# Kernel tuning notes

Hardware: AMD Instinct MI355X
Metric: run time of the kernel (lower is better)

Reference implementation:

```python
import jax, jax.numpy as jnp
import numpy as np

B, S, D = 4, 1024, 1024
H, G = 16, 8            # num_heads, num_query_groups
HD = D // H             # head_dim = 64
E, TOPK, ED = 8, 2, 2 * D   # experts, top_k, expert_dim
GH = D // 2             # gate hidden
EPS = 1e-5


def setup_inputs() -> dict:
    key = jax.random.key(0)
    ks = iter(jax.random.split(key, 32))
    rn = lambda shape, s=0.02: jax.random.normal(next(ks), shape, jnp.float32) * s
    return {
        "x": jax.random.normal(next(ks), (B, S, D), jnp.float32),
        # GQA projections (stored [in, out])
        "wq": rn((D, G * HD)), "bq": jnp.zeros((G * HD,), jnp.float32),
        "wk": rn((D, D)), "bk": jnp.zeros((D,), jnp.float32),
        "wv": rn((D, D)), "bv": jnp.zeros((D,), jnp.float32),
        "wo": rn((D, D)), "bo": jnp.zeros((D,), jnp.float32),
        # LayerNorms
        "ln1_g": jnp.ones((D,), jnp.float32), "ln1_b": jnp.zeros((D,), jnp.float32),
        "ln2_g": jnp.ones((D,), jnp.float32), "ln2_b": jnp.zeros((D,), jnp.float32),
        # MoE gate: Linear(D, D//2) -> ReLU -> Linear(D//2, E)
        "gw1": rn((D, GH)), "gb1": jnp.zeros((GH,), jnp.float32),
        "gw2": rn((GH, E)), "gb2": jnp.zeros((E,), jnp.float32),
        # stacked expert FFNs: Linear(D, ED) -> GELU -> Linear(ED, D)
        "ew1": rn((E, D, ED)), "eb1": jnp.zeros((E, ED), jnp.float32),
        "ew2": rn((E, ED, D)), "eb2": jnp.zeros((E, D), jnp.float32),
    }


def _layernorm(x, g, b):
    mu = jnp.mean(x, axis=-1, keepdims=True)
    var = jnp.var(x, axis=-1, keepdims=True)
    return (x - mu) * jax.lax.rsqrt(var + EPS) * g + b


def _block(x, wq, bq, wk, bk, wv, bv, wo, bo, ln1_g, ln1_b, ln2_g, ln2_b,
           gw1, gb1, gw2, gb2, ew1, eb1, ew2, eb2):
    # --- GQA self-attention (dropout is identity in eval) ---
    h = _layernorm(x, ln1_g, ln1_b)
    q = (h @ wq + bq).reshape(B, S, G, HD).transpose(0, 2, 1, 3)   # [B,G,S,hd]
    k = (h @ wk + bk).reshape(B, S, H, HD).transpose(0, 2, 1, 3)   # [B,H,S,hd]
    v = (h @ wv + bv).reshape(B, S, H, HD).transpose(0, 2, 1, 3)
    q = jnp.repeat(q, H // G, axis=1)                              # repeat_interleave -> [B,H,S,hd]
    scores = jnp.einsum("bhqd,bhkd->bhqk", q, k) * (HD ** -0.5)
    attn = jax.nn.softmax(scores, axis=-1)
    ao = jnp.einsum("bhqk,bhkd->bhqd", attn, v)
    ao = ao.transpose(0, 2, 1, 3).reshape(B, S, D) @ wo + bo
    x = x + ao

    # --- MoE FFN ---
    h2 = _layernorm(x, ln2_g, ln2_b).reshape(-1, D)                # [T,D], T=B*S
    gate_logits = jax.nn.relu(h2 @ gw1 + gb1) @ gw2 + gb2          # [T,E]
    gate_w = jax.nn.softmax(gate_logits, axis=-1)
    top_w, top_i = jax.lax.top_k(gate_w, TOPK)                     # [T,k]
    top_w = jax.nn.softmax(top_w, axis=-1)                         # renormalize among top-k
    combine = jnp.sum(jax.nn.one_hot(top_i, E, dtype=h2.dtype) * top_w[..., None], axis=1)  # [T,E]
    hid = jax.nn.gelu(jnp.einsum("td,edh->teh", h2, ew1) + eb1, approximate=False)          # [T,E,ED]
    expert_out = jnp.einsum("teh,ehd->ted", hid, ew2) + eb2        # [T,E,D]
    moe = jnp.einsum("ted,te->td", expert_out, combine).reshape(B, S, D)
    return x + moe


def reference(x, wq, bq, wk, bk, wv, bv, wo, bo, ln1_g, ln1_b, ln2_g, ln2_b,
              gw1, gb1, gw2, gb2, ew1, eb1, ew2, eb2):
    return _block(x, wq, bq, wk, bk, wv, bv, wo, bo, ln1_g, ln1_b, ln2_g, ln2_b,
                  gw1, gb1, gw2, gb2, ew1, eb1, ew2, eb2)
```

## Files before the change

kernel.cpp:

```cpp
#include <hip/hip_runtime.h>

typedef __bf16 bf16x8 __attribute__((ext_vector_type(8)));
typedef float f32x4 __attribute__((ext_vector_type(4)));
typedef unsigned int u32x4 __attribute__((ext_vector_type(4)));
typedef unsigned int u32x2 __attribute__((ext_vector_type(2)));

#define DEV static __device__ __forceinline__

DEV unsigned short f2bf(float f) {
  unsigned int u = __builtin_bit_cast(unsigned int, f);
  u += 0x7fffu + ((u >> 16) & 1u);
  return (unsigned short)(u >> 16);
}
DEV float bf2f(unsigned int hbits) { return __builtin_bit_cast(float, hbits << 16); }

DEV bf16x8 load_bf8(const unsigned short* p) {
  u32x4 u = *(const u32x4*)p;
  return __builtin_bit_cast(bf16x8, u);
}
DEV void unpack8(u32x4 u, float f[8]) {
  f[0] = bf2f(u.x & 0xffffu); f[1] = bf2f(u.x >> 16);
  f[2] = bf2f(u.y & 0xffffu); f[3] = bf2f(u.y >> 16);
  f[4] = bf2f(u.z & 0xffffu); f[5] = bf2f(u.z >> 16);
  f[6] = bf2f(u.w & 0xffffu); f[7] = bf2f(u.w >> 16);
}
DEV void gload_lds16(const void* g, void* l) {
  __builtin_amdgcn_global_load_lds((const __attribute__((address_space(1))) void*)g,
                                   (__attribute__((address_space(3))) void*)l, 16, 0, 0);
}
DEV f32x4 mfma16(bf16x8 a, bf16x8 b, f32x4 c) {
  return __builtin_amdgcn_mfma_f32_16x16x32_bf16(a, b, c, 0, 0, 0);
}

__global__ __launch_bounds__(256) void cm_transpose(
    const float* __restrict__ src, unsigned short* __restrict__ dst,
    int K, int N, long srcStrideE, long dstStrideE) {
  src += (long)blockIdx.z * srcStrideE;
  dst += (long)blockIdx.z * dstStrideE;
  __shared__ float t[32][33];
  const int n0 = blockIdx.x * 32, k0 = blockIdx.y * 32;
  const int tx = threadIdx.x & 31, ty = threadIdx.x >> 5;
#pragma unroll
  for (int j = 0; j < 4; ++j) {
    int k = k0 + ty + j * 8, n = n0 + tx;
    if (k < K && n < N) t[ty + j * 8][tx] = src[(long)k * N + n];
  }
  __syncthreads();
#pragma unroll
  for (int j = 0; j < 4; ++j) {
    int n = n0 + ty + j * 8, k = k0 + tx;
    if (n < N && k < K) dst[(long)n * K + k] = f2bf(t[tx][ty + j * 8]);
  }
}

__global__ __launch_bounds__(256) void cm_transpose_split(
    const float* __restrict__ src, unsigned short* __restrict__ dhi,
    unsigned short* __restrict__ dlo, int K, int N) {
  __shared__ float t[32][33];
  const int n0 = blockIdx.x * 32, k0 = blockIdx.y * 32;
  const int tx = threadIdx.x & 31, ty = threadIdx.x >> 5;
#pragma unroll
  for (int j = 0; j < 4; ++j) {
    int k = k0 + ty + j * 8, n = n0 + tx;
    if (k < K && n < N) t[ty + j * 8][tx] = src[(long)k * N + n];
  }
  __syncthreads();
#pragma unroll
  for (int j = 0; j < 4; ++j) {
    int n = n0 + ty + j * 8, k = k0 + tx;
    if (n < N && k < K) {
      float v = t[tx][ty + j * 8];
      unsigned short hi = f2bf(v);
      dhi[(long)n * K + k] = hi;
      dlo[(long)n * K + k] = f2bf(v - bf2f(hi));
    }
  }
}

template <bool WLO>
__global__ __launch_bounds__(256) void cm_ln(
    const float* __restrict__ x, const float* __restrict__ g, const float* __restrict__ b,
    unsigned short* __restrict__ ob, unsigned short* __restrict__ olo) {
  const int row = blockIdx.x, tid = threadIdx.x;
  const f32x4 v = *(const f32x4*)(x + (long)row * 1024 + tid * 4);
  float s1 = v[0] + v[1] + v[2] + v[3];
  float s2 = v[0] * v[0] + v[1] * v[1] + v[2] * v[2] + v[3] * v[3];
#pragma unroll
  for (int m = 32; m >= 1; m >>= 1) { s1 += __shfl_xor(s1, m); s2 += __shfl_xor(s2, m); }
  __shared__ float r1[4], r2[4];
  if ((tid & 63) == 0) { r1[tid >> 6] = s1; r2[tid >> 6] = s2; }
  __syncthreads();
  s1 = r1[0] + r1[1] + r1[2] + r1[3];
  s2 = r2[0] + r2[1] + r2[2] + r2[3];
  const float mean = s1 * (1.f / 1024.f);
  const float rs = rsqrtf(s2 * (1.f / 1024.f) - mean * mean + 1e-5f);
  const f32x4 gg = *(const f32x4*)(g + tid * 4);
  const f32x4 bb = *(const f32x4*)(b + tid * 4);
  float o[4];
  unsigned short hi[4];
#pragma unroll
  for (int i = 0; i < 4; ++i) {
    o[i] = (v[i] - mean) * rs * gg[i] + bb[i];
    hi[i] = f2bf(o[i]);
  }
  u32x2 pk;
  pk.x = (unsigned)hi[0] | ((unsigned)hi[1] << 16);
  pk.y = (unsigned)hi[2] | ((unsigned)hi[3] << 16);
  *(u32x2*)(ob + (long)row * 1024 + tid * 4) = pk;
  if (WLO) {
    u32x2 pl;
    pl.x = (unsigned)f2bf(o[0] - bf2f(hi[0])) | ((unsigned)f2bf(o[1] - bf2f(hi[1])) << 16);
    pl.y = (unsigned)f2bf(o[2] - bf2f(hi[2])) | ((unsigned)f2bf(o[3] - bf2f(hi[3])) << 16);
    *(u32x2*)(olo + (long)row * 1024 + tid * 4) = pl;
  }
}

enum { EP_BF16 = 0, EP_RELU = 1, EP_GELU = 2, EP_RES_F32 = 3 };

template <int EPI, int MODE>
__global__ __launch_bounds__(256, 2) void cm_gemm_bt(
    const unsigned short* __restrict__ A, int lda,
    const unsigned short* __restrict__ BT, long btStrideE, int ldb,
    const float* __restrict__ bias, int biasStrideE,
    const float* __restrict__ res,
    void* __restrict__ outp, int ldc,
    int M, int K,
    const int* __restrict__ cnt, const int* __restrict__ offs,
    const int* __restrict__ rowidx) {
  const int z = blockIdx.z;
  int valid = M, rowbase = 0;
  if (MODE > 0) {
    valid = cnt[z];
    if ((int)blockIdx.y * 128 >= valid) return;
    rowbase = offs[z];
    BT += (long)z * btStrideE;
    bias += (long)z * biasStrideE;
  }
  const int tid = threadIdx.x;
  const int brow = blockIdx.y * 128, bcol = blockIdx.x * 128;
  const int wid = tid >> 6, lane = tid & 63;
  const int wr = wid >> 1, wc = wid & 1;
  const int srow0 = tid >> 2, scol = (tid & 3) * 8;

  __shared__ __align__(16) unsigned short As[128 * 32];
  __shared__ __align__(16) unsigned short Bs[128 * 32];

  long asrc[2], bsrc[2];
#pragma unroll
  for (int i = 0; i < 2; ++i) {
    int m = brow + srow0 + i * 64;
    if (MODE == 0) {
      asrc[i] = (long)m * lda;
    } else {
      int p = m < valid ? m : valid - 1;
      if (MODE == 1) asrc[i] = (long)rowidx[z * 4096 + p] * lda;
      else           asrc[i] = (long)(rowbase + p) * lda;
    }
    bsrc[i] = (long)(bcol + srow0 + i * 64) * ldb;
  }

  f32x4 acc[4][4] = {};

  for (int k0 = 0; k0 < K; k0 += 32) {
#pragma unroll
    for (int i = 0; i < 2; ++i) {
      gload_lds16(A + asrc[i] + k0 + scol, &As[(srow0 + i * 64) * 32 + scol]);
      gload_lds16(BT + bsrc[i] + k0 + scol, &Bs[(srow0 + i * 64) * 32 + scol]);
    }
    __syncthreads();
    bf16x8 af[4], bfr[4];
#pragma unroll
    for (int m = 0; m < 4; ++m)
      af[m] = load_bf8(&As[(wr * 64 + m * 16 + (lane & 15)) * 32 + (lane >> 4) * 8]);
#pragma unroll
    for (int n = 0; n < 4; ++n)
      bfr[n] = load_bf8(&Bs[(wc * 64 + n * 16 + (lane & 15)) * 32 + (lane >> 4) * 8]);
#pragma unroll
    for (int m = 0; m < 4; ++m)
#pragma unroll
      for (int n = 0; n < 4; ++n)
        acc[m][n] = mfma16(af[m], bfr[n], acc[m][n]);
    __syncthreads();
  }

#pragma unroll
  for (int m = 0; m < 4; ++m) {
#pragma unroll
    for (int rr = 0; rr < 4; ++rr) {
      const int lrow = brow + wr * 64 + m * 16 + (lane >> 4) * 4 + rr;
      if (MODE > 0 && lrow >= valid) continue;
      const long orow = (long)(rowbase + lrow);
#pragma unroll
      for (int n = 0; n < 4; ++n) {
        const int gcol = bcol + wc * 64 + n * 16 + (lane & 15);
        float vv = acc[m][n][rr] + bias[gcol];
        if constexpr (EPI == EP_RELU) vv = fmaxf(vv, 0.f);
        if constexpr (EPI == EP_GELU) vv = 0.5f * vv * (1.f + erff(vv * 0.70710678f));
        if constexpr (EPI == EP_RES_F32)
          ((float*)outp)[orow * ldc + gcol] = vv + res[orow * ldc + gcol];
        else
          ((unsigned short*)outp)[orow * ldc + gcol] = f2bf(vv);
      }
    }
  }
}

__global__ __launch_bounds__(256, 2) void cm_gemm_gate(
    const unsigned short* __restrict__ Ah, const unsigned short* __restrict__ Al,
    const unsigned short* __restrict__ Bh, const unsigned short* __restrict__ Bl,
    const float* __restrict__ bias, float* __restrict__ C) {
  const int tid = threadIdx.x;
  const int brow = blockIdx.y * 128, bcol = blockIdx.x * 128;
  const int wid = tid >> 6, lane = tid & 63;
  const int wr = wid >> 1, wc = wid & 1;
  const int srow0 = tid >> 2, scol = (tid & 3) * 8;

  __shared__ __align__(16) unsigned short Ash[128 * 32], Asl[128 * 32];
  __shared__ __align__(16) unsigned short Bsh[128 * 32], Bsl[128 * 32];

  f32x4 acc[4][4] = {};

  for (int k0 = 0; k0 < 1024; k0 += 32) {
#pragma unroll
    for (int i = 0; i < 2; ++i) {
      const long ar = (long)(brow + srow0 + i * 64) * 1024 + k0 + scol;
      const long br = (long)(bcol + srow0 + i * 64) * 1024 + k0 + scol;
      const int lo = (srow0 + i * 64) * 32 + scol;
      gload_lds16(Ah + ar, &Ash[lo]);
      gload_lds16(Al + ar, &Asl[lo]);
      gload_lds16(Bh + br, &Bsh[lo]);
      gload_lds16(Bl + br, &Bsl[lo]);
    }
    __syncthreads();
    bf16x8 ah[4], al[4], bh[4], bl[4];
#pragma unroll
    for (int m = 0; m < 4; ++m) {
      const int ro = (wr * 64 + m * 16 + (lane & 15)) * 32 + (lane >> 4) * 8;
      ah[m] = load_bf8(&Ash[ro]); al[m] = load_bf8(&Asl[ro]);
    }
#pragma unroll
    for (int n = 0; n < 4; ++n) {
      const int ro = (wc * 64 + n * 16 + (lane & 15)) * 32 + (lane >> 4) * 8;
      bh[n] = load_bf8(&Bsh[ro]); bl[n] = load_bf8(&Bsl[ro]);
    }
#pragma unroll
    for (int m = 0; m < 4; ++m)
#pragma unroll
      for (int n = 0; n < 4; ++n) {
        acc[m][n] = mfma16(al[m], bh[n], acc[m][n]);
        acc[m][n] = mfma16(ah[m], bl[n], acc[m][n]);
        acc[m][n] = mfma16(ah[m], bh[n], acc[m][n]);
      }
    __syncthreads();
  }

#pragma unroll
  for (int m = 0; m < 4; ++m)
#pragma unroll
    for (int rr = 0; rr < 4; ++rr) {
      const long orow = brow + wr * 64 + m * 16 + (lane >> 4) * 4 + rr;
#pragma unroll
      for (int n = 0; n < 4; ++n) {
        const int gcol = bcol + wc * 64 + n * 16 + (lane & 15);
        C[orow * 512 + gcol] = fmaxf(acc[m][n][rr] + bias[gcol], 0.f);
      }
    }
}

__global__ __launch_bounds__(256) void cm_vtrans(
    const unsigned short* __restrict__ qkv, unsigned short* __restrict__ Vt) {
  const int stile = blockIdx.x, bh = blockIdx.y;
  const int b = bh >> 4, h = bh & 15;
  const int tid = threadIdx.x;
  __shared__ __align__(16) unsigned short t[64][72];
  const int d0 = (tid & 7) * 8, sl = tid >> 3;
#pragma unroll
  for (int i = 0; i < 2; ++i) {
    const int s = sl + i * 32;
    *(u32x4*)&t[s][d0] =
        *(const u32x4*)(qkv + (long)(b * 1024 + stile * 64 + s) * 2560 + 1536 + h * 64 + d0);
  }
  __syncthreads();
  const int s0 = (tid & 7) * 8, dl = tid >> 3;
#pragma unroll
  for (int i = 0; i < 2; ++i) {
    const int d = dl + i * 32;
    unsigned short vals[8];
#pragma unroll
    for (int j = 0; j < 8; ++j) vals[j] = t[s0 + j][d];
    u32x4 u;
    u.x = vals[0] | ((unsigned)vals[1] << 16);
    u.y = vals[2] | ((unsigned)vals[3] << 16);
    u.z = vals[4] | ((unsigned)vals[5] << 16);
    u.w = vals[6] | ((unsigned)vals[7] << 16);
    *(u32x4*)(Vt + (long)(bh * 64 + d) * 1024 + stile * 64 + s0) = u;
  }
}

__global__ __launch_bounds__(256, 2) void cm_attn(
    const unsigned short* __restrict__ qkv,
    const unsigned short* __restrict__ Vt,
    unsigned short* __restrict__ ao) {
  const int qt = blockIdx.x, bh = blockIdx.y;
  const int b = bh >> 4, h = bh & 15, g = h >> 1;
  const int tid = threadIdx.x, wid = tid >> 6, lane = tid & 63;
  const int q0 = qt * 32;

  __shared__ __align__(16) unsigned short sc[32][1032];
  __shared__ float rowrcp[32];

  bf16x8 bq[2][2];
#pragma unroll
  for (int nf = 0; nf < 2; ++nf)
#pragma unroll
    for (int ks = 0; ks < 2; ++ks)
      bq[nf][ks] = load_bf8(qkv + (long)(b * 1024 + q0 + nf * 16 + (lane & 15)) * 2560 +
                            g * 64 + ks * 32 + (lane >> 4) * 8);

#pragma unroll 1
  for (int c = 0; c < 4; ++c) {
    const int kb = wid * 256 + c * 64;
    f32x4 acc[4][2] = {};
#pragma unroll
    for (int ks = 0; ks < 2; ++ks) {
      bf16x8 ak[4];
#pragma unroll
      for (int mf = 0; mf < 4; ++mf)
        ak[mf] = load_bf8(qkv + (long)(b * 1024 + kb + mf * 16 + (lane & 15)) * 2560 +
                          512 + h * 64 + ks * 32 + (lane >> 4) * 8);
#pragma unroll
      for (int mf = 0; mf < 4; ++mf)
#pragma unroll
        for (int nf = 0; nf < 2; ++nf)
          acc[mf][nf] = mfma16(ak[mf], bq[nf][ks], acc[mf][nf]);
    }
#pragma unroll
    for (int mf = 0; mf < 4; ++mf)
#pragma unroll
      for (int nf = 0; nf < 2; ++nf) {
        const int q = nf * 16 + (lane & 15);
        const int key = kb + mf * 16 + (lane >> 4) * 4;
        u32x2 pk;
        pk.x = (unsigned)f2bf(acc[mf][nf][0] * 0.125f) |
               ((unsigned)f2bf(acc[mf][nf][1] * 0.125f) << 16);
        pk.y = (unsigned)f2bf(acc[mf][nf][2] * 0.125f) |
               ((unsigned)f2bf(acc[mf][nf][3] * 0.125f) << 16);
        *(u32x2*)&sc[q][key] = pk;
      }
  }
  __syncthreads();

  {
    const int row = tid >> 3, seg = tid & 7;
    float mx = -1e30f;
#pragma unroll
    for (int i = 0; i < 16; ++i) {
      float f[8];
      unpack8(*(const u32x4*)&sc[row][i * 64 + seg * 8], f);
#pragma unroll
      for (int j = 0; j < 8; ++j) mx = fmaxf(mx, f[j]);
    }
#pragma unroll
    for (int m = 4; m >= 1; m >>= 1) mx = fmaxf(mx, __shfl_xor(mx, m));
    float sum = 0.f;
#pragma unroll 1
    for (int i = 0; i < 16; ++i) {
      float f[8];
      unpack8(*(const u32x4*)&sc[row][i * 64 + seg * 8], f);
      float e[8];
#pragma unroll
      for (int j = 0; j < 8; ++j) { e[j] = __expf(f[j] - mx); sum += e[j]; }
      u32x4 o;
      o.x = (unsigned)f2bf(e[0]) | ((unsigned)f2bf(e[1]) << 16);
      o.y = (unsigned)f2bf(e[2]) | ((unsigned)f2bf(e[3]) << 16);
      o.z = (unsigned)f2bf(e[4]) | ((unsigned)f2bf(e[5]) << 16);
      o.w = (unsigned)f2bf(e[6]) | ((unsigned)f2bf(e[7]) << 16);
      *(u32x4*)&sc[row][i * 64 + seg * 8] = o;
    }
#pragma unroll
    for (int m = 4; m >= 1; m >>= 1) sum += __shfl_xor(sum, m);
    if (seg == 0) rowrcp[row] = 1.f / sum;
  }
  __syncthreads();

  {
    f32x4 acc[2] = {};
    const unsigned short* vtb = Vt + (long)bh * 64 * 1024;
#pragma unroll 4
    for (int k0 = 0; k0 < 1024; k0 += 32) {
      const bf16x8 bv =
          load_bf8(vtb + (long)(wid * 16 + (lane & 15)) * 1024 + k0 + (lane >> 4) * 8);
#pragma unroll
      for (int m = 0; m < 2; ++m) {
        const bf16x8 ap = load_bf8(&sc[m * 16 + (lane & 15)][k0 + (lane >> 4) * 8]);
        acc[m] = mfma16(ap, bv, acc[m]);
      }
    }
#pragma unroll
    for (int m = 0; m < 2; ++m)
#pragma unroll
      for (int rr = 0; rr < 4; ++rr) {
        const int q = m * 16 + (lane >> 4) * 4 + rr;
        const int d = wid * 16 + (lane & 15);
        ao[(long)(b * 1024 + q0 + q) * 1024 + h * 64 + d] = f2bf(acc[m][rr] * rowrcp[q]);
      }
  }
}

__global__ __launch_bounds__(64) void cm_route_pick(
    const float* __restrict__ g1f, const float* __restrict__ gw2, const float* __restrict__ gb2,
    int* __restrict__ pick, int* __restrict__ slot_e, float* __restrict__ rwt) {
  const int t = blockIdx.x, lane = threadIdx.x;
  f32x4 a0 = *(const f32x4*)(g1f + (long)t * 512 + lane * 8);
  f32x4 a1 = *(const f32x4*)(g1f + (long)t * 512 + lane * 8 + 4);
  float logit[8];
#pragma unroll
  for (int e = 0; e < 8; ++e) {
    float s = 0.f;
#pragma unroll
    for (int j = 0; j < 4; ++j) {
      s += a0[j] * gw2[(lane * 8 + j) * 8 + e];
      s += a1[j] * gw2[(lane * 8 + 4 + j) * 8 + e];
    }
#pragma unroll
    for (int m = 32; m >= 1; m >>= 1) s += __shfl_xor(s, m);
    logit[e] = s + gb2[e];
  }
  float mx = logit[0];
#pragma unroll
  for (int e = 1; e < 8; ++e) mx = fmaxf(mx, logit[e]);
  float p[8], sum = 0.f;
#pragma unroll
  for (int e = 0; e < 8; ++e) { p[e] = __expf(logit[e] - mx); sum += p[e]; }
  const float rs = 1.f / sum;
#pragma unroll
  for (int e = 0; e < 8; ++e) p[e] *= rs;
  int i0 = 0;
#pragma unroll
  for (int e = 1; e < 8; ++e) if (p[e] > p[i0]) i0 = e;
  int i1 = (i0 == 0) ? 1 : 0;
#pragma unroll
  for (int e = 0; e < 8; ++e) if (e != i0 && p[e] > p[i1]) i1 = e;
  const float w0 = 1.f / (1.f + __expf(p[i1] - p[i0]));
  if (lane == 0) {
    pick[t] = i0 | (i1 << 8);
    slot_e[t * 2] = i0; slot_e[t * 2 + 1] = i1;
    rwt[t * 2] = w0;    rwt[t * 2 + 1] = 1.f - w0;
  }
}

__global__ __launch_bounds__(256) void cm_route_place(
    const int* __restrict__ pick, int* __restrict__ cnt,
    int* __restrict__ etok, int* __restrict__ slot_p) {
  const int t = blockIdx.x * 256 + threadIdx.x;
  const int lane = threadIdx.x & 63;
  const int pk = pick[t];
  const int p0 = pk & 15, p1 = (pk >> 8) & 15;
  const unsigned long long lt = ((unsigned long long)1 << lane) - 1;
  int my_r0 = 0, my_c0p1 = 0, my_r1 = 0, tot = 0;
#pragma unroll
  for (int e = 0; e < 8; ++e) {
    const unsigned long long m0 = __ballot(p0 == e);
    const unsigned long long m1 = __ballot(p1 == e);
    if (p0 == e) my_r0 = __popcll(m0 & lt);
    if (p1 == e) { my_c0p1 = __popcll(m0); my_r1 = __popcll(m1 & lt); }
    if (lane == e) tot = __popcll(m0) + __popcll(m1);
  }
  int base = 0;
  if (lane < 8 && tot > 0) base = atomicAdd(&cnt[lane], tot);
  const int b0 = __shfl(base, p0);
  const int b1 = __shfl(base, p1);
  const int pos0 = b0 + my_r0;
  const int pos1 = b1 + my_c0p1 + my_r1;
  etok[p0 * 4096 + pos0] = t;
  etok[p1 * 4096 + pos1] = t;
  slot_p[t * 2] = pos0;
  slot_p[t * 2 + 1] = pos1;
}

__global__ void cm_offs(const int* __restrict__ cnt, int* __restrict__ offs) {
  if (threadIdx.x == 0) {
    int s = 0;
#pragma unroll
    for (int e = 0; e < 8; ++e) { offs[e] = s; s += cnt[e]; }
  }
}

__global__ __launch_bounds__(256) void cm_combine(
    const float* __restrict__ x2, const unsigned short* __restrict__ eo,
    const int* __restrict__ slot_e, const int* __restrict__ slot_p,
    const float* __restrict__ rwt, const int* __restrict__ offs,
    float* __restrict__ outp) {
  const int t = blockIdx.x, tid = threadIdx.x;
  const long r0 = (long)(offs[slot_e[t * 2]] + slot_p[t * 2]);
  const long r1 = (long)(offs[slot_e[t * 2 + 1]] + slot_p[t * 2 + 1]);
  const float w0 = rwt[t * 2], w1 = rwt[t * 2 + 1];
  const f32x4 xv = *(const f32x4*)(x2 + (long)t * 1024 + tid * 4);
  u32x2 u0 = *(const u32x2*)(eo + r0 * 1024 + tid * 4);
  u32x2 u1 = *(const u32x2*)(eo + r1 * 1024 + tid * 4);
  f32x4 o;
  o[0] = xv[0] + w0 * bf2f(u0.x & 0xffffu) + w1 * bf2f(u1.x & 0xffffu);
  o[1] = xv[1] + w0 * bf2f(u0.x >> 16) + w1 * bf2f(u1.x >> 16);
  o[2] = xv[2] + w0 * bf2f(u0.y & 0xffffu) + w1 * bf2f(u1.y & 0xffffu);
  o[3] = xv[3] + w0 * bf2f(u0.y >> 16) + w1 * bf2f(u1.y >> 16);
  *(f32x4*)(outp + (long)t * 1024 + tid * 4) = o;
}

extern "C" void kernel_launch(void* const* d_in, const int* in_sizes, int n_in,
                              void* d_out, int out_size, void* d_ws, size_t ws_size,
                              hipStream_t stream) {
  if (n_in < 21) return;
  const float* x    = (const float*)d_in[0];
  const float* wq   = (const float*)d_in[1];
  const float* bq   = (const float*)d_in[2];
  const float* wk   = (const float*)d_in[3];
  const float* bk   = (const float*)d_in[4];
  const float* wv   = (const float*)d_in[5];
  const float* bv   = (const float*)d_in[6];
  const float* wo   = (const float*)d_in[7];
  const float* bo   = (const float*)d_in[8];
  const float* ln1g = (const float*)d_in[9];
  const float* ln1b = (const float*)d_in[10];
  const float* ln2g = (const float*)d_in[11];
  const float* ln2b = (const float*)d_in[12];
  const float* gw1  = (const float*)d_in[13];
  const float* gb1  = (const float*)d_in[14];
  const float* gw2  = (const float*)d_in[15];
  const float* gb2  = (const float*)d_in[16];
  const float* ew1  = (const float*)d_in[17];
  const float* eb1  = (const float*)d_in[18];
  const float* ew2  = (const float*)d_in[19];
  const float* eb2  = (const float*)d_in[20];
  float* outp = (float*)d_out;

  char* ws = (char*)d_ws;
  size_t off = 0;
  auto carve = [&](size_t bytes) -> char* {
    char* p = ws + off;
    off += (bytes + 255) & ~(size_t)255;
    return p;
  };
  unsigned short* wqkvT = (unsigned short*)carve(2560l * 1024 * 2);
  unsigned short* woT   = (unsigned short*)carve(1024l * 1024 * 2);
  unsigned short* gw1hT = (unsigned short*)carve(512l * 1024 * 2);
  unsigned short* gw1lT = (unsigned short*)carve(512l * 1024 * 2);
  unsigned short* ew1T  = (unsigned short*)carve(8l * 2048 * 1024 * 2);
  unsigned short* ew2T  = (unsigned short*)carve(8l * 1024 * 2048 * 2);
  float* bqkv           = (float*)carve(2560 * 4);
  unsigned short* hbuf  = (unsigned short*)carve(4096l * 1024 * 2);
  unsigned short* qkvl  = (unsigned short*)carve(4096l * 2560 * 2);
  unsigned short* Vt    = (unsigned short*)carve(4096l * 1024 * 2);
  unsigned short* ao    = (unsigned short*)carve(4096l * 1024 * 2);
  unsigned short* h2    = (unsigned short*)carve(4096l * 1024 * 2);
  unsigned short* h2lo  = (unsigned short*)carve(4096l * 1024 * 2);
  int* cnt              = (int*)carve(8 * 4);
  int* offs             = (int*)carve(8 * 4);
  int* etok             = (int*)carve(8l * 4096 * 4);
  int* slot_e           = (int*)carve(8192 * 4);
  int* slot_p           = (int*)carve(8192 * 4);
  float* rwt            = (float*)carve(8192 * 4);
  int* pick             = (int*)carve(4096 * 4);
  unsigned short* hid   = (unsigned short*)carve(8192l * 2048 * 2);
  unsigned short* eo    = (unsigned short*)carve(8192l * 1024 * 2);
  if (off > ws_size) return;
  float* x2 = outp;
  float* g1f = (float*)Vt;

  (void)hipMemsetAsync(cnt, 0, 8 * 4, stream);
  (void)hipMemcpyAsync(bqkv, (const void*)bq, 512 * 4, hipMemcpyDeviceToDevice, stream);
  (void)hipMemcpyAsync(bqkv + 512, (const void*)bk, 1024 * 4, hipMemcpyDeviceToDevice, stream);
  (void)hipMemcpyAsync(bqkv + 1536, (const void*)bv, 1024 * 4, hipMemcpyDeviceToDevice, stream);

  cm_transpose<<<dim3(16, 32, 1), 256, 0, stream>>>(wq, wqkvT, 1024, 512, 0l, 0l);
  cm_transpose<<<dim3(32, 32, 1), 256, 0, stream>>>(wk, wqkvT + 512l * 1024, 1024, 1024, 0l, 0l);
  cm_transpose<<<dim3(32, 32, 1), 256, 0, stream>>>(wv, wqkvT + 1536l * 1024, 1024, 1024, 0l, 0l);
  cm_transpose<<<dim3(32, 32, 1), 256, 0, stream>>>(wo, woT, 1024, 1024, 0l, 0l);
  cm_transpose_split<<<dim3(16, 32, 1), 256, 0, stream>>>(gw1, gw1hT, gw1lT, 1024, 512);
  cm_transpose<<<dim3(64, 32, 8), 256, 0, stream>>>(ew1, ew1T, 1024, 2048, 1024l * 2048, 2048l * 1024);
  cm_transpose<<<dim3(32, 64, 8), 256, 0, stream>>>(ew2, ew2T, 2048, 1024, 2048l * 1024, 1024l * 2048);

  cm_ln<false><<<4096, 256, 0, stream>>>(x, ln1g, ln1b, hbuf, nullptr);
  cm_gemm_bt<EP_BF16, 0><<<dim3(20, 32, 1), 256, 0, stream>>>(
      hbuf, 1024, wqkvT, 0l, 1024, bqkv, 0, nullptr, qkvl, 2560, 4096, 1024,
      nullptr, nullptr, nullptr);
  cm_vtrans<<<dim3(16, 64, 1), 256, 0, stream>>>(qkvl, Vt);
  cm_attn<<<dim3(32, 64, 1), 256, 0, stream>>>(qkvl, Vt, ao);
  cm_gemm_bt<EP_RES_F32, 0><<<dim3(8, 32, 1), 256, 0, stream>>>(
      ao, 1024, woT, 0l, 1024, bo, 0, x, x2, 1024, 4096, 1024,
      nullptr, nullptr, nullptr);
  cm_ln<true><<<4096, 256, 0, stream>>>(x2, ln2g, ln2b, h2, h2lo);

  cm_gemm_gate<<<dim3(4, 32, 1), 256, 0, stream>>>(h2, h2lo, gw1hT, gw1lT, gb1, g1f);
  cm_route_pick<<<4096, 64, 0, stream>>>(g1f, gw2, gb2, pick, slot_e, rwt);
  cm_route_place<<<16, 256, 0, stream>>>(pick, cnt, etok, slot_p);
  cm_offs<<<1, 64, 0, stream>>>(cnt, offs);

  cm_gemm_bt<EP_GELU, 1><<<dim3(16, 32, 8), 256, 0, stream>>>(
      h2, 1024, ew1T, 2048l * 1024, 1024, eb1, 2048, nullptr, hid, 2048, 4096, 1024,
      cnt, offs, etok);
  cm_gemm_bt<EP_BF16, 2><<<dim3(8, 32, 8), 256, 0, stream>>>(
      hid, 2048, ew2T, 1024l * 2048, 2048, eb2, 1024, nullptr, eo, 1024, 4096, 2048,
      cnt, offs, nullptr);
  cm_combine<<<4096, 256, 0, stream>>>(x2, eo, slot_e, slot_p, rwt, offs, outp);
}
```

Baseline: 490.0 us.

## Double-buffer LDS tiles and remap workgroups across XCDs in GEMM kernel

Switches the generic GEMM kernel to double-buffered shared-memory tiles, so global-to-LDS loads for the next K-step are issued while the current step's MFMAs run. It also remaps the flat workgroup index so consecutive logical tiles land on the same XCD, aiming to improve L2 reuse of A/B tiles. This doubles LDS use per block, which may reduce occupancy, and it relies on the existing end-of-loop barrier for correctness of buffer reuse.

```diff
diff --git a/kernel.cpp b/kernel.cpp
--- a/kernel.cpp
+++ b/kernel.cpp
@@ -127,23 +127,36 @@
     int M, int K,
     const int* __restrict__ cnt, const int* __restrict__ offs,
     const int* __restrict__ rowidx) {
-  const int z = blockIdx.z;
+  const int gx = gridDim.x, gy = gridDim.y;
+  const int nwg = gx * gy * (int)gridDim.z;
+  int flat = (int)blockIdx.x + gx * ((int)blockIdx.y + gy * (int)blockIdx.z);
+  {
+    const int q = nwg >> 3, r = nwg & 7, xcd = flat & 7, idx = flat >> 3;
+    flat = (xcd < r ? xcd * (q + 1) : r * (q + 1) + (xcd - r) * q) + idx;
+  }
+  const int bx = flat % gx;
+  const int rest = flat / gx;
+  const int by = rest % gy;
+  const int z = rest / gy;
+
   int valid = M, rowbase = 0;
+  const unsigned short* Bp = BT;
+  const float* biasp = bias;
   if (MODE > 0) {
     valid = cnt[z];
-    if ((int)blockIdx.y * 128 >= valid) return;
+    if (by * 128 >= valid) return;
     rowbase = offs[z];
-    BT += (long)z * btStrideE;
-    bias += (long)z * biasStrideE;
+    Bp += (long)z * btStrideE;
+    biasp += (long)z * biasStrideE;
   }
   const int tid = threadIdx.x;
-  const int brow = blockIdx.y * 128, bcol = blockIdx.x * 128;
+  const int brow = by * 128, bcol = bx * 128;
   const int wid = tid >> 6, lane = tid & 63;
   const int wr = wid >> 1, wc = wid & 1;
   const int srow0 = tid >> 2, scol = (tid & 3) * 8;
 
-  __shared__ __align__(16) unsigned short As[128 * 32];
-  __shared__ __align__(16) unsigned short Bs[128 * 32];
+  __shared__ __align__(16) unsigned short As[2][128 * 32];
+  __shared__ __align__(16) unsigned short Bs[2][128 * 32];
 
   long asrc[2], bsrc[2];
 #pragma unroll
@@ -158,23 +171,34 @@
     }
     bsrc[i] = (long)(bcol + srow0 + i * 64) * ldb;
   }
+  const int ldst = srow0 * 32 + scol;
+  const int ldst2 = ldst + 64 * 32;
 
   f32x4 acc[4][4] = {};
-
-  for (int k0 = 0; k0 < K; k0 += 32) {
-#pragma unroll
-    for (int i = 0; i < 2; ++i) {
-      gload_lds16(A + asrc[i] + k0 + scol, &As[(srow0 + i * 64) * 32 + scol]);
-      gload_lds16(BT + bsrc[i] + k0 + scol, &Bs[(srow0 + i * 64) * 32 + scol]);
-    }
-    __syncthreads();
+  const int nt = K >> 5;
+
+  gload_lds16(A + asrc[0] + scol, &As[0][ldst]);
+  gload_lds16(A + asrc[1] + scol, &As[0][ldst2]);
+  gload_lds16(Bp + bsrc[0] + scol, &Bs[0][ldst]);
+  gload_lds16(Bp + bsrc[1] + scol, &Bs[0][ldst2]);
+  __syncthreads();
+
+  for (int t = 0; t < nt; ++t) {
+    const int cur = t & 1;
+    if (t + 1 < nt) {
+      const int k0 = (t + 1) << 5;
+      gload_lds16(A + asrc[0] + k0 + scol, &As[cur ^ 1][ldst]);
+      gload_lds16(A + asrc[1] + k0 + scol, &As[cur ^ 1][ldst2]);
+      gload_lds16(Bp + bsrc[0] + k0 + scol, &Bs[cur ^ 1][ldst]);
+      gload_lds16(Bp + bsrc[1] + k0 + scol, &Bs[cur ^ 1][ldst2]);
+    }
     bf16x8 af[4], bfr[4];
 #pragma unroll
     for (int m = 0; m < 4; ++m)
-      af[m] = load_bf8(&As[(wr * 64 + m * 16 + (lane & 15)) * 32 + (lane >> 4) * 8]);
+      af[m] = load_bf8(&As[cur][(wr * 64 + m * 16 + (lane & 15)) * 32 + (lane >> 4) * 8]);
 #pragma unroll
     for (int n = 0; n < 4; ++n)
-      bfr[n] = load_bf8(&Bs[(wc * 64 + n * 16 + (lane & 15)) * 32 + (lane >> 4) * 8]);
+      bfr[n] = load_bf8(&Bs[cur][(wc * 64 + n * 16 + (lane & 15)) * 32 + (lane >> 4) * 8]);
 #pragma unroll
     for (int m = 0; m < 4; ++m)
 #pragma unroll
@@ -193,7 +217,7 @@
 #pragma unroll
       for (int n = 0; n < 4; ++n) {
         const int gcol = bcol + wc * 64 + n * 16 + (lane & 15);
-        float vv = acc[m][n][rr] + bias[gcol];
+        float vv = acc[m][n][rr] + biasp[gcol];
         if constexpr (EPI == EP_RELU) vv = fmaxf(vv, 0.f);
         if constexpr (EPI == EP_GELU) vv = 0.5f * vv * (1.f + erff(vv * 0.70710678f));
         if constexpr (EPI == EP_RES_F32)
```

New measurement: 492.5 us. No clear change (+0.5%).
